# Kernel optimization log

Hardware: AMD Instinct MI355X
Metric: run time of the kernel (lower is better)

Reference implementation:

```python
import jax, jax.numpy as jnp
import numpy as np

N, B, I = 64, 32, 1
EMBED, ACT, DETER, STOCH, HIDDEN = 1536, 16, 2048, 512, 1024
EPS = 1e-5


def _ln(x, g, b):
    m = jnp.mean(x, -1, keepdims=True)
    v = jnp.mean((x - m) ** 2, -1, keepdims=True)
    return (x - m) / jnp.sqrt(v + EPS) * g + b


def setup_inputs() -> dict:
    key = jax.random.key(0)
    ks = jax.random.split(key, 24)
    s = 0.02
    d = {
        "embed": jax.random.normal(ks[0], (N, B, EMBED), jnp.float32),
        "action": jax.random.normal(ks[1], (N, B, ACT), jnp.float32),
        "reset": jnp.zeros((N, B), jnp.bool_),
        "h0": jnp.zeros((B * I, DETER), jnp.float32),
        "z0": jnp.zeros((B * I, STOCH), jnp.float32),
        "noises": jax.random.normal(ks[2], (N, B, I, STOCH), jnp.float32),
        # params
        "W_z": jax.random.normal(ks[3], (HIDDEN, STOCH)) * s,
        "b_z": jnp.zeros((HIDDEN,)),
        "W_a": jax.random.normal(ks[4], (HIDDEN, ACT)) * s,
        "ln_in_g": jnp.ones((HIDDEN,)), "ln_in_b": jnp.zeros((HIDDEN,)),
        "gru_Wih": jax.random.normal(ks[5], (3 * DETER, HIDDEN)) * s,
        "gru_Whh": jax.random.normal(ks[6], (3 * DETER, DETER)) * s,
        "gru_bih": jnp.zeros((3 * DETER,)), "gru_bhh": jnp.zeros((3 * DETER,)),
        "W_ph": jax.random.normal(ks[7], (HIDDEN, DETER)) * s,
        "b_ph": jnp.zeros((HIDDEN,)),
        "W_pe": jax.random.normal(ks[8], (HIDDEN, EMBED)) * s,
        "ln_post_g": jnp.ones((HIDDEN,)), "ln_post_b": jnp.zeros((HIDDEN,)),
        "W_post": jax.random.normal(ks[9], (2 * STOCH, HIDDEN)) * s,
        "b_post": jnp.zeros((2 * STOCH,)),
        "W_prh": jax.random.normal(ks[10], (HIDDEN, DETER)) * s,
        "b_prh": jnp.zeros((HIDDEN,)),
        "ln_pr_g": jnp.ones((HIDDEN,)), "ln_pr_b": jnp.zeros((HIDDEN,)),
        "W_pr": jax.random.normal(ks[11], (2 * STOCH, HIDDEN)) * s,
        "b_pr": jnp.zeros((2 * STOCH,)),
    }
    return d


def _core(embed, action, reset, h0, z0, noises,
          W_z, b_z, W_a, ln_in_g, ln_in_b,
          gru_Wih, gru_Whh, gru_bih, gru_bhh,
          W_ph, b_ph, W_pe, ln_post_g, ln_post_b, W_post, b_post,
          W_prh, b_prh, ln_pr_g, ln_pr_b, W_pr, b_pr):
    n, b = embed.shape[:2]
    # expand to (n, b*I, .) ; I == 1
    embeds = embed.reshape(n, b * I, -1)
    actions = action.reshape(n, b * I, -1)
    masks = (~reset).astype(jnp.float32).reshape(n, b * I, 1)
    noise = noises.reshape(n, b * I, -1)

    def step(carry, xs):
        h, z = carry
        e_t, a_t, m_t, n_t = xs
        h = h * m_t
        z = z * m_t
        x = z @ W_z.T + b_z + a_t @ W_a.T
        za = jax.nn.elu(_ln(x, ln_in_g, ln_in_b))
        # torch GRUCell
        gi = za @ gru_Wih.T + gru_bih
        gh = h @ gru_Whh.T + gru_bhh
        gi_r, gi_u, gi_n = jnp.split(gi, 3, -1)
        gh_r, gh_u, gh_n = jnp.split(gh, 3, -1)
        r = jax.nn.sigmoid(gi_r + gh_r)
        u = jax.nn.sigmoid(gi_u + gh_u)
        cand = jnp.tanh(gi_n + r * gh_n)
        h_new = (1.0 - u) * cand + u * h
        x = h_new @ W_ph.T + b_ph + e_t @ W_pe.T
        post_in = jax.nn.elu(_ln(x, ln_post_g, ln_post_b))
        post = post_in @ W_post.T + b_post
        mean, std_raw = jnp.split(post, 2, -1)
        std = jax.nn.softplus(std_raw) + 0.1
        sample = mean + std * n_t
        return (h_new, sample), (post, h_new, sample)

    (h_last, z_last), (posts, states_h, samples) = jax.lax.scan(
        step, (h0, z0), (embeds, actions, masks, noise))

    # batch prior over all h
    x = states_h @ W_prh.T + b_prh
    x = jax.nn.elu(_ln(x, ln_pr_g, ln_pr_b))
    priors = x @ W_pr.T + b_pr
    features = jnp.concatenate([states_h, samples], -1)

    rs = lambda t: t.reshape(n, b, I, -1)
    return rs(priors), rs(posts), rs(samples), rs(features), h_last, z_last


def reference(embed, action, reset, h0, z0, noises,
              W_z, b_z, W_a, ln_in_g, ln_in_b,
              gru_Wih, gru_Whh, gru_bih, gru_bhh,
              W_ph, b_ph, W_pe, ln_post_g, ln_post_b, W_post, b_post,
              W_prh, b_prh, ln_pr_g, ln_pr_b, W_pr, b_pr):
    return _core(embed, action, reset, h0, z0, noises,
                 W_z, b_z, W_a, ln_in_g, ln_in_b,
                 gru_Wih, gru_Whh, gru_bih, gru_bhh,
                 W_ph, b_ph, W_pe, ln_post_g, ln_post_b, W_post, b_post,
                 W_prh, b_prh, ln_pr_g, ln_pr_b, W_pr, b_pr)
```

## Files before the change

### kernel.cpp

```cpp
#include <hip/hip_runtime.h>
#include <hip/hip_bf16.h>
#include <stdint.h>

#define NSTEP 64
#define BATCH 32
#define EMBED_D 1536
#define ACT_D 16
#define DETER 2048
#define STOCH 512
#define HIDDEN 1024
#define FEAT 2560
#define NBLK 256

typedef __attribute__((ext_vector_type(8))) short bf16x8;
typedef __attribute__((ext_vector_type(4))) float f32x4;

#define MFMA16 __builtin_amdgcn_mfma_f32_16x16x32_bf16
#define AGENT __HIP_MEMORY_SCOPE_AGENT

__device__ __forceinline__ float eluf(float x) { return x > 0.f ? x : expf(x) - 1.f; }
__device__ __forceinline__ float sigf(float x) { return 1.f / (1.f + expf(-x)); }
__device__ __forceinline__ unsigned short f2bf(float f) {
    __hip_bfloat16 h = __float2bfloat16(f);
    return __builtin_bit_cast(unsigned short, h);
}
__device__ __forceinline__ float bf2f(unsigned short u) {
    unsigned v = ((unsigned)u) << 16;
    return __builtin_bit_cast(float, v);
}

__device__ __forceinline__ void stc_u32(unsigned* p, unsigned v) {
    __hip_atomic_store(p, v, __ATOMIC_RELAXED, AGENT);
}
__device__ __forceinline__ void stc_u64(unsigned long long* p, unsigned long long v) {
    __hip_atomic_store(p, v, __ATOMIC_RELAXED, AGENT);
}
__device__ __forceinline__ unsigned long long ldc_u64(const unsigned long long* p) {
    return __hip_atomic_load(p, __ATOMIC_RELAXED, AGENT);
}
__device__ __forceinline__ float ldc_f32(const float* p) {
    return __hip_atomic_load(p, __ATOMIC_RELAXED, AGENT);
}
__device__ __forceinline__ int ldc_i32(const int* p) {
    return __hip_atomic_load(p, __ATOMIC_RELAXED, AGENT);
}
__device__ __forceinline__ void stc_i32(int* p, int v) {
    __hip_atomic_store(p, v, __ATOMIC_RELAXED, AGENT);
}
__device__ __forceinline__ bf16x8 ldc_bf8(const unsigned short* p) {
    union { unsigned long long q[2]; bf16x8 v; } u;
    u.q[0] = ldc_u64((const unsigned long long*)p);
    u.q[1] = ldc_u64((const unsigned long long*)(p + 4));
    return u.v;
}
__device__ __forceinline__ ushort4 ldc_us4(const unsigned short* p) {
    unsigned long long q = ldc_u64((const unsigned long long*)p);
    return __builtin_bit_cast(ushort4, q);
}

__device__ __forceinline__ void gbar2(int* flags, int* release, int epoch) {
    asm volatile("s_waitcnt vmcnt(0)" ::: "memory");
    __syncthreads();
    if (blockIdx.x == 0) {
        int tid = threadIdx.x;
        if (tid >= 1 && tid < NBLK) {
            while (ldc_i32(&flags[tid * 32]) < epoch) __builtin_amdgcn_s_sleep(4);
        }
        asm volatile("" ::: "memory");
        __syncthreads();
        if (tid == 0) stc_i32(release, epoch);
    } else {
        if (threadIdx.x == 0) {
            stc_i32(&flags[blockIdx.x * 32], epoch);
            while (ldc_i32(release) < epoch) __builtin_amdgcn_s_sleep(4);
        }
        asm volatile("" ::: "memory");
        __syncthreads();
    }
}

__global__ __launch_bounds__(256) void k_cvt_all(
    const float* __restrict__ s0, unsigned short* __restrict__ d0,
    const float* __restrict__ s1, unsigned short* __restrict__ d1,
    const float* __restrict__ s2, unsigned short* __restrict__ d2,
    const float* __restrict__ s3, unsigned short* __restrict__ d3,
    const float* __restrict__ s4, unsigned short* __restrict__ d4)
{
    long long e = ((long long)blockIdx.x * 256 + threadIdx.x) * 4;
    const float* src; unsigned short* dst; long long off;
    if (e < 524288)        { src = s0; dst = d0; off = e; }
    else if (e < 6815744)  { src = s1; dst = d1; off = e - 524288; }
    else if (e < 19398656) { src = s2; dst = d2; off = e - 6815744; }
    else if (e < 21495808) { src = s3; dst = d3; off = e - 19398656; }
    else if (e < 22544384) { src = s4; dst = d4; off = e - 21495808; }
    else return;
    float4 v = *reinterpret_cast<const float4*>(src + off);
    ushort4 o;
    o.x = f2bf(v.x); o.y = f2bf(v.y); o.z = f2bf(v.z); o.w = f2bf(v.w);
    *reinterpret_cast<ushort4*>(dst + off) = o;
}

__global__ __launch_bounds__(256) void k_setup(
    const float* __restrict__ h0, const float* __restrict__ z0,
    const uint8_t* __restrict__ reset0,
    float* __restrict__ h0m, unsigned short* __restrict__ h16m0,
    unsigned short* __restrict__ z16m, int* __restrict__ flags)
{
    int gid = blockIdx.x * 256 + threadIdx.x;
    int idx = gid * 4;
    if (idx < BATCH * DETER) {
        int b = idx >> 11;
        float m = reset0[b] ? 0.f : 1.f;
        float4 v = *reinterpret_cast<const float4*>(h0 + idx);
        v.x *= m; v.y *= m; v.z *= m; v.w *= m;
        *reinterpret_cast<float4*>(h0m + idx) = v;
        ushort4 o;
        o.x = f2bf(v.x); o.y = f2bf(v.y); o.z = f2bf(v.z); o.w = f2bf(v.w);
        *reinterpret_cast<ushort4*>(h16m0 + idx) = o;
    } else if (idx < BATCH * DETER + BATCH * STOCH) {
        int zi = idx - BATCH * DETER;
        int b = zi >> 9;
        float m = reset0[b] ? 0.f : 1.f;
        float4 v = *reinterpret_cast<const float4*>(z0 + zi);
        ushort4 o;
        o.x = f2bf(v.x * m); o.y = f2bf(v.y * m); o.z = f2bf(v.z * m); o.w = f2bf(v.w * m);
        *reinterpret_cast<ushort4*>(z16m + zi) = o;
    }
    if (gid < 8224) flags[gid] = 0;
}

__global__ __launch_bounds__(256) void k_preA(
    const float* __restrict__ action, const float* __restrict__ Wa,
    const float* __restrict__ bz, float* __restrict__ preA)
{
    __shared__ float al[16];
    int r = blockIdx.x, t = threadIdx.x;
    if (t < 16) al[t] = action[r * 16 + t];
    __syncthreads();
#pragma unroll
    for (int c = 0; c < 4; ++c) {
        int j = t + c * 256;
        const float* wr = Wa + j * 16;
        float s = bz[j];
#pragma unroll
        for (int k = 0; k < 16; ++k) s += al[k] * wr[k];
        preA[(size_t)r * 1024 + j] = s;
    }
}

__global__ __launch_bounds__(256) void gemm_mfma(
    const float* __restrict__ A, int lda,
    const float* __restrict__ B, int ldb,
    const float* __restrict__ bias,
    float* __restrict__ C, int ldc, int K)
{
    __shared__ unsigned short Alds[64 * 72];
    __shared__ unsigned short Blds[64 * 72];
    int t = threadIdx.x;
    int nb = blockIdx.x, mb = blockIdx.y;
    int w = t >> 6, l = t & 63, l15 = l & 15, kg = l >> 4;
    f32x4 acc[4] = {{0,0,0,0},{0,0,0,0},{0,0,0,0},{0,0,0,0}};
    int srow = t >> 2, skq = (t & 3) * 16;
    const float* Asrc = A + (size_t)(mb * 64 + srow) * lda + skq;
    const float* Bsrc = B + (size_t)(nb * 64 + srow) * ldb + skq;
    unsigned short* Adst = &Alds[srow * 72 + skq];
    unsigned short* Bdst = &Blds[srow * 72 + skq];
    for (int kt = 0; kt < K; kt += 64) {
        __syncthreads();
#pragma unroll
        for (int c = 0; c < 16; c += 4) {
            float4 va = *reinterpret_cast<const float4*>(Asrc + kt + c);
            float4 vb = *reinterpret_cast<const float4*>(Bsrc + kt + c);
            ushort4 oa, ob;
            oa.x = f2bf(va.x); oa.y = f2bf(va.y); oa.z = f2bf(va.z); oa.w = f2bf(va.w);
            ob.x = f2bf(vb.x); ob.y = f2bf(vb.y); ob.z = f2bf(vb.z); ob.w = f2bf(vb.w);
            *reinterpret_cast<ushort4*>(Adst + c) = oa;
            *reinterpret_cast<ushort4*>(Bdst + c) = ob;
        }
        __syncthreads();
#pragma unroll
        for (int ks = 0; ks < 2; ks++) {
            bf16x8 a = *reinterpret_cast<const bf16x8*>(&Alds[(w * 16 + l15) * 72 + ks * 32 + kg * 8]);
#pragma unroll
            for (int nt = 0; nt < 4; nt++) {
                bf16x8 b = *reinterpret_cast<const bf16x8*>(&Blds[(nt * 16 + l15) * 72 + ks * 32 + kg * 8]);
                acc[nt] = MFMA16(a, b, acc[nt], 0, 0, 0);
            }
        }
    }
#pragma unroll
    for (int nt = 0; nt < 4; nt++) {
        int n = nb * 64 + nt * 16 + l15;
        float bv = bias[n];
#pragma unroll
        for (int i = 0; i < 4; i++) {
            C[(size_t)(mb * 64 + w * 16 + kg * 4 + i) * ldc + n] = acc[nt][i] + bv;
        }
    }
}

__global__ __launch_bounds__(256) void ln_elu_rows(
    float* __restrict__ X, const float* __restrict__ g, const float* __restrict__ bb)
{
    __shared__ float sbuf[256], qbuf[256];
    int r = blockIdx.x, t = threadIdx.x;
    float* row = X + (size_t)r * HIDDEN;
    float4 v = reinterpret_cast<const float4*>(row)[t];
    sbuf[t] = (v.x + v.y) + (v.z + v.w);
    qbuf[t] = (v.x * v.x + v.y * v.y) + (v.z * v.z + v.w * v.w);
    __syncthreads();
    for (int off = 128; off > 0; off >>= 1) {
        if (t < off) { sbuf[t] += sbuf[t + off]; qbuf[t] += qbuf[t + off]; }
        __syncthreads();
    }
    float mean = sbuf[0] / HIDDEN;
    float var = qbuf[0] / HIDDEN - mean * mean;
    float rstd = rsqrtf(var + 1e-5f);
    float4 gg = reinterpret_cast<const float4*>(g)[t];
    float4 bv = reinterpret_cast<const float4*>(bb)[t];
    float4 o;
    o.x = eluf((v.x - mean) * rstd * gg.x + bv.x);
    o.y = eluf((v.y - mean) * rstd * gg.y + bv.y);
    o.z = eluf((v.z - mean) * rstd * gg.z + bv.z);
    o.w = eluf((v.w - mean) * rstd * gg.w + bv.w);
    reinterpret_cast<float4*>(row)[t] = o;
}

__global__ __launch_bounds__(256) void k_copy_last(
    const float* __restrict__ feat63, const float* __restrict__ samp63,
    float* __restrict__ hlast, float* __restrict__ zlast)
{
    int i = blockIdx.x * 256 + threadIdx.x;
    if (i < BATCH * DETER) {
        int b = i / DETER, k = i % DETER;
        hlast[i] = feat63[(size_t)b * FEAT + k];
    }
    if (i < BATCH * STOCH) zlast[i] = samp63[i];
}

struct ScanArgs {
    const unsigned short *Wz16, *Wih16, *Whh16, *Wph16, *Wpo16;
    const float *bih, *bhh, *b_post;
    const float *ln_in_g, *ln_in_b, *ln_post_g, *ln_post_b;
    const float *h0m;
    const uint8_t *reset;
    const float *noises;
    float *postsPreA;
    float *priorsPreE;
    float *samples;
    float *feats;
    unsigned short *z16m, *x1b, *x2b, *h16u, *h16m0, *h16m1;
    float *x1parts, *x2parts;
    int *flags, *release;
};

__device__ __forceinline__ void ln_stats(const float* __restrict__ parts, float* stat, int tid) {
    if (tid < 32) {
        float s = 0.f, q = 0.f;
        for (int i = 0; i < 64; ++i) {
            union { unsigned long long u; float f[2]; } c;
            c.u = ldc_u64((const unsigned long long*)(parts + (size_t)(i * 32 + tid) * 2));
            s += c.f[0]; q += c.f[1];
        }
        float mean = s * (1.f / 1024.f);
        float var = q * (1.f / 1024.f) - mean * mean;
        stat[tid] = mean;
        stat[32 + tid] = rsqrtf(var + 1e-5f);
    }
}

__device__ __forceinline__ void ln_fill(unsigned short* Asm, const unsigned short* __restrict__ src,
                                        const float* __restrict__ g, const float* __restrict__ bb,
                                        const float* stat, int tid) {
    int row = tid & 31, kb = (tid >> 5) * 128;
    float mean = stat[row], rstd = stat[32 + row];
#pragma unroll 4
    for (int c = 0; c < 16; ++c) {
        int k = kb + c * 8;
        ushort4 u0 = ldc_us4(src + (size_t)row * 1024 + k);
        ushort4 u1 = ldc_us4(src + (size_t)row * 1024 + k + 4);
        float4 g0 = *reinterpret_cast<const float4*>(g + k);
        float4 g1 = *reinterpret_cast<const float4*>(g + k + 4);
        float4 b0 = *reinterpret_cast<const float4*>(bb + k);
        float4 b1 = *reinterpret_cast<const float4*>(bb + k + 4);
        ushort4 o0, o1;
        o0.x = f2bf(eluf((bf2f(u0.x) - mean) * rstd * g0.x + b0.x));
        o0.y = f2bf(eluf((bf2f(u0.y) - mean) * rstd * g0.y + b0.y));
        o0.z = f2bf(eluf((bf2f(u0.z) - mean) * rstd * g0.z + b0.z));
        o0.w = f2bf(eluf((bf2f(u0.w) - mean) * rstd * g0.w + b0.w));
        o1.x = f2bf(eluf((bf2f(u1.x) - mean) * rstd * g1.x + b1.x));
        o1.y = f2bf(eluf((bf2f(u1.y) - mean) * rstd * g1.y + b1.y));
        o1.z = f2bf(eluf((bf2f(u1.z) - mean) * rstd * g1.z + b1.z));
        o1.w = f2bf(eluf((bf2f(u1.w) - mean) * rstd * g1.w + b1.w));
        *reinterpret_cast<ushort4*>(Asm + row * 1032 + k) = o0;
        *reinterpret_cast<ushort4*>(Asm + row * 1032 + k + 4) = o1;
    }
}

__global__ __launch_bounds__(256, 1) void k_scan(ScanArgs a) {
    __shared__ char smem[74752];
    unsigned short* Asm = (unsigned short*)smem;
    float* cbuf = (float*)(smem + 66048);
    float* stat = (float*)(smem + 66048 + 8192);

    const int bid = blockIdx.x;
    const int tid = threadIdx.x;
    const int w = tid >> 6, l = tid & 63, l15 = l & 15, kg = l >> 4;
    int epoch = 0;

    for (int t = 0; t < NSTEP; ++t) {
        const float* preA_t = a.postsPreA + (size_t)t * 32768;
        const float* preE_t = a.priorsPreE + (size_t)t * 32768;
        float* posts_t = a.postsPreA + (size_t)t * 32768;
        float* samples_t = a.samples + (size_t)t * 16384;
        float* feats_t = a.feats + (size_t)t * 81920;
        const float* featsPrev = a.feats + (size_t)(t - 1) * 81920;
        const unsigned short* h16cur = (t & 1) ? a.h16m1 : a.h16m0;
        unsigned short* h16nxt = (t & 1) ? a.h16m0 : a.h16m1;

        if (bid < 64) {
            int j0 = bid * 16;
            const unsigned short* A0 = a.z16m + l15 * 512 + w * 128 + kg * 8;
            const unsigned short* A1 = A0 + 16 * 512;
            const unsigned short* Bp = a.Wz16 + (size_t)(j0 + l15) * 512 + w * 128 + kg * 8;
            f32x4 c0 = {0,0,0,0}, c1 = {0,0,0,0};
#pragma unroll
            for (int ks = 0; ks < 4; ++ks) {
                bf16x8 b = *reinterpret_cast<const bf16x8*>(Bp + ks * 32);
                c0 = MFMA16(ldc_bf8(A0 + ks * 32), b, c0, 0, 0, 0);
                c1 = MFMA16(ldc_bf8(A1 + ks * 32), b, c1, 0, 0, 0);
            }
#pragma unroll
            for (int i = 0; i < 4; ++i) {
                cbuf[w * 512 + (kg * 4 + i) * 16 + l15] = c0[i];
                cbuf[w * 512 + (16 + kg * 4 + i) * 16 + l15] = c1[i];
            }
            __syncthreads();
            int r = tid >> 3, c2 = (tid & 7) * 2;
            int base = r * 16 + c2;
            float v0 = cbuf[base] + cbuf[512 + base] + cbuf[1024 + base] + cbuf[1536 + base]
                     + preA_t[r * 1024 + j0 + c2];
            float v1 = cbuf[base + 1] + cbuf[512 + base + 1] + cbuf[1024 + base + 1] + cbuf[1536 + base + 1]
                     + preA_t[r * 1024 + j0 + c2 + 1];
            unsigned short u0 = f2bf(v0), u1 = f2bf(v1);
            stc_u32((unsigned*)(a.x1b + (size_t)r * 1024 + j0 + c2),
                    (unsigned)u0 | ((unsigned)u1 << 16));
            float w0 = bf2f(u0), w1 = bf2f(u1);
            float s = w0 + w1, q = w0 * w0 + w1 * w1;
            s += __shfl_xor(s, 1); q += __shfl_xor(q, 1);
            s += __shfl_xor(s, 2); q += __shfl_xor(q, 2);
            s += __shfl_xor(s, 4); q += __shfl_xor(q, 4);
            if ((tid & 7) == 0) {
                union { float f[2]; unsigned long long u; } pu;
                pu.f[0] = s; pu.f[1] = q;
                stc_u64((unsigned long long*)(a.x1parts + ((size_t)bid * 32 + r) * 2), pu.u);
            }
        }
        epoch++; gbar2(a.flags, a.release, epoch);

        if (bid < 128) {
            int j0 = bid * 16;
            ln_stats(a.x1parts, stat, tid);
            __syncthreads();
            ln_fill(Asm, a.x1b, a.ln_in_g, a.ln_in_b, stat, tid);
            __syncthreads();
            bool isI = (w < 2);
            int mt = w & 1;
            f32x4 cr = {0,0,0,0}, cu = {0,0,0,0}, cn = {0,0,0,0};
            if (isI) {
                const unsigned short* ap = Asm + (mt * 16 + l15) * 1032 + kg * 8;
                const unsigned short* br = a.Wih16 + (size_t)(j0 + l15) * 1024 + kg * 8;
                const unsigned short* bu = br + (size_t)2048 * 1024;
                const unsigned short* bn = bu + (size_t)2048 * 1024;
#pragma unroll 8
                for (int ks = 0; ks < 32; ++ks) {
                    bf16x8 av = *reinterpret_cast<const bf16x8*>(ap + ks * 32);
                    cr = MFMA16(av, *reinterpret_cast<const bf16x8*>(br + ks * 32), cr, 0, 0, 0);
                    cu = MFMA16(av, *reinterpret_cast<const bf16x8*>(bu + ks * 32), cu, 0, 0, 0);
                    cn = MFMA16(av, *reinterpret_cast<const bf16x8*>(bn + ks * 32), cn, 0, 0, 0);
                }
            } else {
                const unsigned short* ap = h16cur + (size_t)(mt * 16 + l15) * 2048 + kg * 8;
                const unsigned short* br = a.Whh16 + (size_t)(j0 + l15) * 2048 + kg * 8;
                const unsigned short* bu = br + (size_t)2048 * 2048;
                const unsigned short* bn = bu + (size_t)2048 * 2048;
#pragma unroll 8
                for (int ks = 0; ks < 64; ++ks) {
                    bf16x8 av = ldc_bf8(ap + ks * 32);
                    cr = MFMA16(av, *reinterpret_cast<const bf16x8*>(br + ks * 32), cr, 0, 0, 0);
                    cu = MFMA16(av, *reinterpret_cast<const bf16x8*>(bu + ks * 32), cu, 0, 0, 0);
                    cn = MFMA16(av, *reinterpret_cast<const bf16x8*>(bn + ks * 32), cn, 0, 0, 0);
                }
#pragma unroll
                for (int i = 0; i < 4; ++i) {
                    cbuf[((mt * 3 + 0) * 16 + kg * 4 + i) * 16 + l15] = cr[i];
                    cbuf[((mt * 3 + 1) * 16 + kg * 4 + i) * 16 + l15] = cu[i];
                    cbuf[((mt * 3 + 2) * 16 + kg * 4 + i) * 16 + l15] = cn[i];
                }
            }
            __syncthreads();
            if (isI) {
                int j = j0 + l15;
                float bihr = a.bih[j], bihu = a.bih[j + 2048], bihn = a.bih[j + 4096];
                float bhhr = a.bhh[j], bhhu = a.bhh[j + 2048], bhhn = a.bhh[j + 4096];
#pragma unroll
                for (int i = 0; i < 4; ++i) {
                    int b = mt * 16 + kg * 4 + i;
                    float gr = cr[i] + bihr, gu = cu[i] + bihu, gn = cn[i] + bihn;
                    float hr = cbuf[((mt * 3 + 0) * 16 + kg * 4 + i) * 16 + l15] + bhhr;
                    float hu = cbuf[((mt * 3 + 1) * 16 + kg * 4 + i) * 16 + l15] + bhhu;
                    float hn = cbuf[((mt * 3 + 2) * 16 + kg * 4 + i) * 16 + l15] + bhhn;
                    float r = sigf(gr + hr), u = sigf(gu + hu);
                    float cand = tanhf(gn + r * hn);
                    float m = a.reset[t * 32 + b] ? 0.f : 1.f;
                    float hpv = (t == 0) ? a.h0m[b * 2048 + j]
                                         : ldc_f32(featsPrev + (size_t)b * 2560 + j);
                    float hnew = (1.f - u) * cand + u * (m * hpv);
                    cbuf[1536 + b * 16 + l15] = hnew;
                }
            }
            __syncthreads();
            {
                int b = tid >> 3, c2 = (tid & 7) * 2;
                float h0v = cbuf[1536 + b * 16 + c2], h1v = cbuf[1536 + b * 16 + c2 + 1];
                int j = j0 + c2;
                union { float f[2]; unsigned long long u; } fu;
                fu.f[0] = h0v; fu.f[1] = h1v;
                stc_u64((unsigned long long*)(feats_t + (size_t)b * 2560 + j), fu.u);
                unsigned short g0 = f2bf(h0v), g1 = f2bf(h1v);
                stc_u32((unsigned*)(a.h16u + (size_t)b * 2048 + j),
                        (unsigned)g0 | ((unsigned)g1 << 16));
                float mn = (t < 63) ? (a.reset[(t + 1) * 32 + b] ? 0.f : 1.f) : 1.f;
                unsigned short n0 = f2bf(h0v * mn), n1 = f2bf(h1v * mn);
                stc_u32((unsigned*)(h16nxt + (size_t)b * 2048 + j),
                        (unsigned)n0 | ((unsigned)n1 << 16));
            }
        }
        epoch++; gbar2(a.flags, a.release, epoch);

        if (bid < 64) {
            int j0 = bid * 16;
            const unsigned short* A0 = a.h16u + l15 * 2048 + w * 512 + kg * 8;
            const unsigned short* A1 = A0 + 16 * 2048;
            const unsigned short* Bp = a.Wph16 + (size_t)(j0 + l15) * 2048 + w * 512 + kg * 8;
            f32x4 c0 = {0,0,0,0}, c1 = {0,0,0,0};
#pragma unroll 8
            for (int ks = 0; ks < 16; ++ks) {
                bf16x8 b = *reinterpret_cast<const bf16x8*>(Bp + ks * 32);
                c0 = MFMA16(ldc_bf8(A0 + ks * 32), b, c0, 0, 0, 0);
                c1 = MFMA16(ldc_bf8(A1 + ks * 32), b, c1, 0, 0, 0);
            }
#pragma unroll
            for (int i = 0; i < 4; ++i) {
                cbuf[w * 512 + (kg * 4 + i) * 16 + l15] = c0[i];
                cbuf[w * 512 + (16 + kg * 4 + i) * 16 + l15] = c1[i];
            }
            __syncthreads();
            int r = tid >> 3, c2 = (tid & 7) * 2;
            int base = r * 16 + c2;
            float v0 = cbuf[base] + cbuf[512 + base] + cbuf[1024 + base] + cbuf[1536 + base]
                     + preE_t[r * 1024 + j0 + c2];
            float v1 = cbuf[base + 1] + cbuf[512 + base + 1] + cbuf[1024 + base + 1] + cbuf[1536 + base + 1]
                     + preE_t[r * 1024 + j0 + c2 + 1];
            unsigned short u0 = f2bf(v0), u1 = f2bf(v1);
            stc_u32((unsigned*)(a.x2b + (size_t)r * 1024 + j0 + c2),
                    (unsigned)u0 | ((unsigned)u1 << 16));
            float w0 = bf2f(u0), w1 = bf2f(u1);
            float s = w0 + w1, q = w0 * w0 + w1 * w1;
            s += __shfl_xor(s, 1); q += __shfl_xor(q, 1);
            s += __shfl_xor(s, 2); q += __shfl_xor(q, 2);
            s += __shfl_xor(s, 4); q += __shfl_xor(q, 4);
            if ((tid & 7) == 0) {
                union { float f[2]; unsigned long long u; } pu;
                pu.f[0] = s; pu.f[1] = q;
                stc_u64((unsigned long long*)(a.x2parts + ((size_t)bid * 32 + r) * 2), pu.u);
            }
        }
        epoch++; gbar2(a.flags, a.release, epoch);

        if (bid < 32) {
            int j0 = bid * 16;
            ln_stats(a.x2parts, stat, tid);
            __syncthreads();
            ln_fill(Asm, a.x2b, a.ln_post_g, a.ln_post_b, stat, tid);
            __syncthreads();
            int tile = w >> 1, mt = w & 1;
            const unsigned short* ap = Asm + (mt * 16 + l15) * 1032 + kg * 8;
            int n = (tile == 0) ? (j0 + l15) : (512 + j0 + l15);
            const unsigned short* Bp = a.Wpo16 + (size_t)n * 1024 + kg * 8;
            f32x4 c = {0,0,0,0};
#pragma unroll 8
            for (int ks = 0; ks < 32; ++ks) {
                c = MFMA16(*reinterpret_cast<const bf16x8*>(ap + ks * 32),
                           *reinterpret_cast<const bf16x8*>(Bp + ks * 32), c, 0, 0, 0);
            }
#pragma unroll
            for (int i = 0; i < 4; ++i)
                cbuf[(tile * 2 + mt) * 256 + (kg * 4 + i) * 16 + l15] = c[i];
            __syncthreads();
            int b = tid >> 3, c2 = (tid & 7) * 2;
            int j = j0 + c2;
            int ib = (b >> 4) * 256 + (b & 15) * 16;
            float pm0 = cbuf[ib + c2] + a.b_post[j];
            float pm1 = cbuf[ib + c2 + 1] + a.b_post[j + 1];
            float ps0 = cbuf[512 + ib + c2] + a.b_post[512 + j];
            float ps1 = cbuf[512 + ib + c2 + 1] + a.b_post[512 + j + 1];
            posts_t[(size_t)b * 1024 + j] = pm0;
            posts_t[(size_t)b * 1024 + j + 1] = pm1;
            posts_t[(size_t)b * 1024 + 512 + j] = ps0;
            posts_t[(size_t)b * 1024 + 512 + j + 1] = ps1;
            float sp0 = fmaxf(ps0, 0.f) + log1pf(expf(-fabsf(ps0)));
            float sp1 = fmaxf(ps1, 0.f) + log1pf(expf(-fabsf(ps1)));
            float n0v = a.noises[(size_t)t * 16384 + b * 512 + j];
            float n1v = a.noises[(size_t)t * 16384 + b * 512 + j + 1];
            float smp0 = pm0 + (sp0 + 0.1f) * n0v;
            float smp1 = pm1 + (sp1 + 0.1f) * n1v;
            samples_t[(size_t)b * 512 + j] = smp0;
            samples_t[(size_t)b * 512 + j + 1] = smp1;
            feats_t[(size_t)b * 2560 + 2048 + j] = smp0;
            feats_t[(size_t)b * 2560 + 2048 + j + 1] = smp1;
            float mn = (t < 63) ? (a.reset[(t + 1) * 32 + b] ? 0.f : 1.f) : 1.f;
            unsigned short z0_ = f2bf(smp0 * mn), z1_ = f2bf(smp1 * mn);
            stc_u32((unsigned*)(a.z16m + (size_t)b * 512 + j),
                    (unsigned)z0_ | ((unsigned)z1_ << 16));
        }
        epoch++; gbar2(a.flags, a.release, epoch);
    }
}

#define WS_WZ16   ((size_t)0)
#define WS_WIH16  ((size_t)1048576)
#define WS_WHH16  ((size_t)13631488)
#define WS_WPH16  ((size_t)38797312)
#define WS_WPO16  ((size_t)42991616)
#define WS_Z16M   ((size_t)45088768)
#define WS_H16M0  ((size_t)45121536)
#define WS_H16M1  ((size_t)45252608)
#define WS_H16U   ((size_t)45383680)
#define WS_H0M    ((size_t)45514752)
#define WS_X1B    ((size_t)45776896)
#define WS_X2B    ((size_t)45842432)
#define WS_X1P    ((size_t)45907968)
#define WS_X2P    ((size_t)45924352)
#define WS_FLAGS  ((size_t)45940736)
#define WS_REL    ((size_t)45973504)
#define WS_PRX    WS_WIH16

extern "C" void kernel_launch(void* const* d_in, const int* in_sizes, int n_in,
                              void* d_out, int out_size, void* d_ws, size_t ws_size,
                              hipStream_t stream)
{
    (void)in_sizes; (void)n_in; (void)out_size; (void)ws_size;
    const float*   embed  = (const float*)d_in[0];
    const float*   action = (const float*)d_in[1];
    const uint8_t* reset  = (const uint8_t*)d_in[2];
    const float*   h0     = (const float*)d_in[3];
    const float*   z0     = (const float*)d_in[4];
    const float*   noises = (const float*)d_in[5];
    const float*   W_z    = (const float*)d_in[6];
    const float*   b_z    = (const float*)d_in[7];
    const float*   W_a    = (const float*)d_in[8];
    const float*   ln_in_g = (const float*)d_in[9];
    const float*   ln_in_b = (const float*)d_in[10];
    const float*   Wih    = (const float*)d_in[11];
    const float*   Whh    = (const float*)d_in[12];
    const float*   bih    = (const float*)d_in[13];
    const float*   bhh    = (const float*)d_in[14];
    const float*   W_ph   = (const float*)d_in[15];
    const float*   b_ph   = (const float*)d_in[16];
    const float*   W_pe   = (const float*)d_in[17];
    const float*   ln_post_g = (const float*)d_in[18];
    const float*   ln_post_b = (const float*)d_in[19];
    const float*   W_post = (const float*)d_in[20];
    const float*   b_post = (const float*)d_in[21];
    const float*   W_prh  = (const float*)d_in[22];
    const float*   b_prh  = (const float*)d_in[23];
    const float*   ln_pr_g = (const float*)d_in[24];
    const float*   ln_pr_b = (const float*)d_in[25];
    const float*   W_pr   = (const float*)d_in[26];
    const float*   b_pr   = (const float*)d_in[27];

    float* out     = (float*)d_out;
    float* priors  = out;
    float* posts   = out + 2097152;
    float* samples = out + 4194304;
    float* feats   = out + 5242880;
    float* hlast   = out + 10485760;
    float* zlast   = out + 10551296;

    char* ws = (char*)d_ws;
    unsigned short* Wz16  = (unsigned short*)(ws + WS_WZ16);
    unsigned short* Wih16 = (unsigned short*)(ws + WS_WIH16);
    unsigned short* Whh16 = (unsigned short*)(ws + WS_WHH16);
    unsigned short* Wph16 = (unsigned short*)(ws + WS_WPH16);
    unsigned short* Wpo16 = (unsigned short*)(ws + WS_WPO16);
    unsigned short* z16m  = (unsigned short*)(ws + WS_Z16M);
    unsigned short* h16m0 = (unsigned short*)(ws + WS_H16M0);
    unsigned short* h16m1 = (unsigned short*)(ws + WS_H16M1);
    unsigned short* h16u  = (unsigned short*)(ws + WS_H16U);
    float*          h0m   = (float*)(ws + WS_H0M);
    unsigned short* x1b   = (unsigned short*)(ws + WS_X1B);
    unsigned short* x2b   = (unsigned short*)(ws + WS_X2B);
    float*          x1p   = (float*)(ws + WS_X1P);
    float*          x2p   = (float*)(ws + WS_X2P);
    int*            flags = (int*)(ws + WS_FLAGS);
    int*            release = (int*)(ws + WS_REL);
    float*          prx   = (float*)(ws + WS_PRX);

    dim3 blk(256);

    k_cvt_all<<<dim3(22016), blk, 0, stream>>>(W_z, Wz16, Wih, Wih16, Whh, Whh16,
                                               W_ph, Wph16, W_post, Wpo16);
    k_setup<<<dim3(80), blk, 0, stream>>>(h0, z0, reset, h0m, h16m0, z16m, flags);

    k_preA<<<dim3(2048), blk, 0, stream>>>(action, W_a, b_z, posts);
    gemm_mfma<<<dim3(16, 32), blk, 0, stream>>>(embed, EMBED_D, W_pe, EMBED_D, b_ph,
                                                priors, HIDDEN, EMBED_D);

    ScanArgs sa;
    sa.Wz16 = Wz16; sa.Wih16 = Wih16; sa.Whh16 = Whh16; sa.Wph16 = Wph16; sa.Wpo16 = Wpo16;
    sa.bih = bih; sa.bhh = bhh; sa.b_post = b_post;
    sa.ln_in_g = ln_in_g; sa.ln_in_b = ln_in_b; sa.ln_post_g = ln_post_g; sa.ln_post_b = ln_post_b;
    sa.h0m = h0m; sa.reset = reset; sa.noises = noises;
    sa.postsPreA = posts; sa.priorsPreE = priors; sa.samples = samples; sa.feats = feats;
    sa.z16m = z16m; sa.x1b = x1b; sa.x2b = x2b; sa.h16u = h16u;
    sa.h16m0 = h16m0; sa.h16m1 = h16m1;
    sa.x1parts = x1p; sa.x2parts = x2p;
    sa.flags = flags; sa.release = release;
    void* kp[] = { (void*)&sa };
    hipLaunchCooperativeKernel((const void*)k_scan, dim3(NBLK), blk, kp, 0, stream);

    gemm_mfma<<<dim3(16, 32), blk, 0, stream>>>(feats, FEAT, W_prh, DETER, b_prh,
                                                prx, HIDDEN, DETER);
    ln_elu_rows<<<dim3(2048), blk, 0, stream>>>(prx, ln_pr_g, ln_pr_b);
    gemm_mfma<<<dim3(16, 32), blk, 0, stream>>>(prx, HIDDEN, W_pr, HIDDEN, b_pr,
                                                priors, HIDDEN, HIDDEN);

    k_copy_last<<<dim3(256), blk, 0, stream>>>(
        feats + (size_t)(NSTEP - 1) * BATCH * FEAT,
        samples + (size_t)(NSTEP - 1) * BATCH * STOCH,
        hlast, zlast);
}
```

Baseline: 4.744 ms.

## Store recurrent GRU and posterior weights as scaled FP8, dequantize in loop

Converts Wih, Whh and Wph to e4m3 FP8 with a fixed ×1024 scale instead of bf16. Inside the persistent scan kernel the FP8 bytes are expanded to bf16 before each MFMA, and the outputs are rescaled. This halves the bytes streamed per recurrent step, which matters because the scan re-reads these weights every step. The cost is extra conversion ALU work and FP8 quantization error on the weights, which may hurt accuracy against the fp32 reference.

Result: slower. 5.478 ms (+15.5%).

```diff
diff --git a/kernel.cpp b/kernel.cpp
--- a/kernel.cpp
+++ b/kernel.cpp
@@ -1,5 +1,6 @@
 #include <hip/hip_runtime.h>
 #include <hip/hip_bf16.h>
+#include <hip/hip_fp8.h>
 #include <stdint.h>
 
 #define NSTEP 64
@@ -17,6 +18,7 @@
 
 #define MFMA16 __builtin_amdgcn_mfma_f32_16x16x32_bf16
 #define AGENT __HIP_MEMORY_SCOPE_AGENT
+#define INV8 (1.0f / 1024.0f)
 
 __device__ __forceinline__ float eluf(float x) { return x > 0.f ? x : expf(x) - 1.f; }
 __device__ __forceinline__ float sigf(float x) { return 1.f / (1.f + expf(-x)); }
@@ -27,6 +29,39 @@
 __device__ __forceinline__ float bf2f(unsigned short u) {
     unsigned v = ((unsigned)u) << 16;
     return __builtin_bit_cast(float, v);
+}
+
+template <int SEL>
+__device__ __forceinline__ float fp8_to_f32(unsigned u) {
+#if __has_builtin(__builtin_amdgcn_cvt_f32_fp8)
+    return __builtin_amdgcn_cvt_f32_fp8(u, SEL);
+#else
+    __hip_fp8_e4m3 q; q.__x = (unsigned char)(u >> (SEL * 8));
+    return (float)q;
+#endif
+}
+__device__ __forceinline__ unsigned char f32_to_fp8(float x) {
+    x = fminf(fmaxf(x, -448.f), 448.f);
+#if __has_builtin(__builtin_amdgcn_cvt_pk_fp8_f32)
+    int r = __builtin_amdgcn_cvt_pk_fp8_f32(x, x, 0, false);
+    return (unsigned char)(r & 0xff);
+#else
+    __hip_fp8_e4m3 q(x);
+    return q.__x;
+#endif
+}
+__device__ __forceinline__ bf16x8 dq8(const unsigned char* p) {
+    uint2 d = *reinterpret_cast<const uint2*>(p);
+    union { unsigned short s[8]; bf16x8 o; } u;
+    u.s[0] = f2bf(fp8_to_f32<0>(d.x));
+    u.s[1] = f2bf(fp8_to_f32<1>(d.x));
+    u.s[2] = f2bf(fp8_to_f32<2>(d.x));
+    u.s[3] = f2bf(fp8_to_f32<3>(d.x));
+    u.s[4] = f2bf(fp8_to_f32<0>(d.y));
+    u.s[5] = f2bf(fp8_to_f32<1>(d.y));
+    u.s[6] = f2bf(fp8_to_f32<2>(d.y));
+    u.s[7] = f2bf(fp8_to_f32<3>(d.y));
+    return u.o;
 }
 
 __device__ __forceinline__ void stc_u32(unsigned* p, unsigned v) {
@@ -80,24 +115,36 @@
 }
 
 __global__ __launch_bounds__(256) void k_cvt_all(
-    const float* __restrict__ s0, unsigned short* __restrict__ d0,
-    const float* __restrict__ s1, unsigned short* __restrict__ d1,
-    const float* __restrict__ s2, unsigned short* __restrict__ d2,
-    const float* __restrict__ s3, unsigned short* __restrict__ d3,
-    const float* __restrict__ s4, unsigned short* __restrict__ d4)
+    const float* __restrict__ wz, unsigned short* __restrict__ wz16,
+    const float* __restrict__ wpo, unsigned short* __restrict__ wpo16,
+    const float* __restrict__ wih, unsigned char* __restrict__ wih8,
+    const float* __restrict__ whh, unsigned char* __restrict__ whh8,
+    const float* __restrict__ wph, unsigned char* __restrict__ wph8)
 {
     long long e = ((long long)blockIdx.x * 256 + threadIdx.x) * 4;
-    const float* src; unsigned short* dst; long long off;
-    if (e < 524288)        { src = s0; dst = d0; off = e; }
-    else if (e < 6815744)  { src = s1; dst = d1; off = e - 524288; }
-    else if (e < 19398656) { src = s2; dst = d2; off = e - 6815744; }
-    else if (e < 21495808) { src = s3; dst = d3; off = e - 19398656; }
-    else if (e < 22544384) { src = s4; dst = d4; off = e - 21495808; }
-    else return;
-    float4 v = *reinterpret_cast<const float4*>(src + off);
-    ushort4 o;
-    o.x = f2bf(v.x); o.y = f2bf(v.y); o.z = f2bf(v.z); o.w = f2bf(v.w);
-    *reinterpret_cast<ushort4*>(dst + off) = o;
+    if (e < 1572864) {
+        const float* src; unsigned short* dst; long long off;
+        if (e < 524288) { src = wz;  dst = wz16;  off = e; }
+        else            { src = wpo; dst = wpo16; off = e - 524288; }
+        float4 v = *reinterpret_cast<const float4*>(src + off);
+        ushort4 o;
+        o.x = f2bf(v.x); o.y = f2bf(v.y); o.z = f2bf(v.z); o.w = f2bf(v.w);
+        *reinterpret_cast<ushort4*>(dst + off) = o;
+    } else {
+        long long f = e - 1572864;
+        const float* src; unsigned char* dst; long long off;
+        if (f < 6291456)        { src = wih; dst = wih8; off = f; }
+        else if (f < 18874368)  { src = whh; dst = whh8; off = f - 6291456; }
+        else if (f < 20971520)  { src = wph; dst = wph8; off = f - 18874368; }
+        else return;
+        float4 v = *reinterpret_cast<const float4*>(src + off);
+        uchar4 o;
+        o.x = f32_to_fp8(v.x * 1024.f);
+        o.y = f32_to_fp8(v.y * 1024.f);
+        o.z = f32_to_fp8(v.z * 1024.f);
+        o.w = f32_to_fp8(v.w * 1024.f);
+        *reinterpret_cast<uchar4*>(dst + off) = o;
+    }
 }
 
 __global__ __launch_bounds__(256) void k_setup(
@@ -239,7 +286,8 @@
 }
 
 struct ScanArgs {
-    const unsigned short *Wz16, *Wih16, *Whh16, *Wph16, *Wpo16;
+    const unsigned short *Wz16, *Wpo16;
+    const unsigned char *Wih8, *Whh8, *Wph8;
     const float *bih, *bhh, *b_post;
     const float *ln_in_g, *ln_in_b, *ln_post_g, *ln_post_b;
     const float *h0m;
@@ -369,27 +417,27 @@
             f32x4 cr = {0,0,0,0}, cu = {0,0,0,0}, cn = {0,0,0,0};
             if (isI) {
                 const unsigned short* ap = Asm + (mt * 16 + l15) * 1032 + kg * 8;
-                const unsigned short* br = a.Wih16 + (size_t)(j0 + l15) * 1024 + kg * 8;
-                const unsigned short* bu = br + (size_t)2048 * 1024;
-                const unsigned short* bn = bu + (size_t)2048 * 1024;
+                const unsigned char* br = a.Wih8 + (size_t)(j0 + l15) * 1024 + kg * 8;
+                const unsigned char* bu = br + (size_t)2048 * 1024;
+                const unsigned char* bn = bu + (size_t)2048 * 1024;
 #pragma unroll 8
                 for (int ks = 0; ks < 32; ++ks) {
                     bf16x8 av = *reinterpret_cast<const bf16x8*>(ap + ks * 32);
-                    cr = MFMA16(av, *reinterpret_cast<const bf16x8*>(br + ks * 32), cr, 0, 0, 0);
-                    cu = MFMA16(av, *reinterpret_cast<const bf16x8*>(bu + ks * 32), cu, 0, 0, 0);
-                    cn = MFMA16(av, *reinterpret_cast<const bf16x8*>(bn + ks * 32), cn, 0, 0, 0);
+                    cr = MFMA16(av, dq8(br + ks * 32), cr, 0, 0, 0);
+                    cu = MFMA16(av, dq8(bu + ks * 32), cu, 0, 0, 0);
+                    cn = MFMA16(av, dq8(bn + ks * 32), cn, 0, 0, 0);
                 }
             } else {
                 const unsigned short* ap = h16cur + (size_t)(mt * 16 + l15) * 2048 + kg * 8;
-                const unsigned short* br = a.Whh16 + (size_t)(j0 + l15) * 2048 + kg * 8;
-                const unsigned short* bu = br + (size_t)2048 * 2048;
-                const unsigned short* bn = bu + (size_t)2048 * 2048;
+                const unsigned char* br = a.Whh8 + (size_t)(j0 + l15) * 2048 + kg * 8;
+                const unsigned char* bu = br + (size_t)2048 * 2048;
+                const unsigned char* bn = bu + (size_t)2048 * 2048;
 #pragma unroll 8
                 for (int ks = 0; ks < 64; ++ks) {
                     bf16x8 av = ldc_bf8(ap + ks * 32);
-                    cr = MFMA16(av, *reinterpret_cast<const bf16x8*>(br + ks * 32), cr, 0, 0, 0);
-                    cu = MFMA16(av, *reinterpret_cast<const bf16x8*>(bu + ks * 32), cu, 0, 0, 0);
-                    cn = MFMA16(av, *reinterpret_cast<const bf16x8*>(bn + ks * 32), cn, 0, 0, 0);
+                    cr = MFMA16(av, dq8(br + ks * 32), cr, 0, 0, 0);
+                    cu = MFMA16(av, dq8(bu + ks * 32), cu, 0, 0, 0);
+                    cn = MFMA16(av, dq8(bn + ks * 32), cn, 0, 0, 0);
                 }
 #pragma unroll
                 for (int i = 0; i < 4; ++i) {
@@ -406,10 +454,12 @@
 #pragma unroll
                 for (int i = 0; i < 4; ++i) {
                     int b = mt * 16 + kg * 4 + i;
-                    float gr = cr[i] + bihr, gu = cu[i] + bihu, gn = cn[i] + bihn;
-                    float hr = cbuf[((mt * 3 + 0) * 16 + kg * 4 + i) * 16 + l15] + bhhr;
-                    float hu = cbuf[((mt * 3 + 1) * 16 + kg * 4 + i) * 16 + l15] + bhhu;
-                    float hn = cbuf[((mt * 3 + 2) * 16 + kg * 4 + i) * 16 + l15] + bhhn;
+                    float gr = cr[i] * INV8 + bihr;
+                    float gu = cu[i] * INV8 + bihu;
+                    float gn = cn[i] * INV8 + bihn;
+                    float hr = cbuf[((mt * 3 + 0) * 16 + kg * 4 + i) * 16 + l15] * INV8 + bhhr;
+                    float hu = cbuf[((mt * 3 + 1) * 16 + kg * 4 + i) * 16 + l15] * INV8 + bhhu;
+                    float hn = cbuf[((mt * 3 + 2) * 16 + kg * 4 + i) * 16 + l15] * INV8 + bhhn;
                     float r = sigf(gr + hr), u = sigf(gu + hu);
                     float cand = tanhf(gn + r * hn);
                     float m = a.reset[t * 32 + b] ? 0.f : 1.f;
@@ -442,11 +492,11 @@
             int j0 = bid * 16;
             const unsigned short* A0 = a.h16u + l15 * 2048 + w * 512 + kg * 8;
             const unsigned short* A1 = A0 + 16 * 2048;
-            const unsigned short* Bp = a.Wph16 + (size_t)(j0 + l15) * 2048 + w * 512 + kg * 8;
+            const unsigned char* Bp = a.Wph8 + (size_t)(j0 + l15) * 2048 + w * 512 + kg * 8;
             f32x4 c0 = {0,0,0,0}, c1 = {0,0,0,0};
 #pragma unroll 8
             for (int ks = 0; ks < 16; ++ks) {
-                bf16x8 b = *reinterpret_cast<const bf16x8*>(Bp + ks * 32);
+                bf16x8 b = dq8(Bp + ks * 32);
                 c0 = MFMA16(ldc_bf8(A0 + ks * 32), b, c0, 0, 0, 0);
                 c1 = MFMA16(ldc_bf8(A1 + ks * 32), b, c1, 0, 0, 0);
             }
@@ -458,9 +508,9 @@
             __syncthreads();
             int r = tid >> 3, c2 = (tid & 7) * 2;
             int base = r * 16 + c2;
-            float v0 = cbuf[base] + cbuf[512 + base] + cbuf[1024 + base] + cbuf[1536 + base]
+            float v0 = (cbuf[base] + cbuf[512 + base] + cbuf[1024 + base] + cbuf[1536 + base]) * INV8
                      + preE_t[r * 1024 + j0 + c2];
-            float v1 = cbuf[base + 1] + cbuf[512 + base + 1] + cbuf[1024 + base + 1] + cbuf[1536 + base + 1]
+            float v1 = (cbuf[base + 1] + cbuf[512 + base + 1] + cbuf[1024 + base + 1] + cbuf[1536 + base + 1]) * INV8
                      + preE_t[r * 1024 + j0 + c2 + 1];
             unsigned short u0 = f2bf(v0), u1 = f2bf(v1);
             stc_u32((unsigned*)(a.x2b + (size_t)r * 1024 + j0 + c2),
@@ -529,22 +579,22 @@
 }
 
 #define WS_WZ16   ((size_t)0)
-#define WS_WIH16  ((size_t)1048576)
-#define WS_WHH16  ((size_t)13631488)
-#define WS_WPH16  ((size_t)38797312)
-#define WS_WPO16  ((size_t)42991616)
-#define WS_Z16M   ((size_t)45088768)
-#define WS_H16M0  ((size_t)45121536)
-#define WS_H16M1  ((size_t)45252608)
-#define WS_H16U   ((size_t)45383680)
-#define WS_H0M    ((size_t)45514752)
-#define WS_X1B    ((size_t)45776896)
-#define WS_X2B    ((size_t)45842432)
-#define WS_X1P    ((size_t)45907968)
-#define WS_X2P    ((size_t)45924352)
-#define WS_FLAGS  ((size_t)45940736)
-#define WS_REL    ((size_t)45973504)
-#define WS_PRX    WS_WIH16
+#define WS_WIH8   ((size_t)1048576)
+#define WS_WHH8   ((size_t)7340032)
+#define WS_WPH8   ((size_t)19922944)
+#define WS_WPO16  ((size_t)22020096)
+#define WS_Z16M   ((size_t)24117248)
+#define WS_H16M0  ((size_t)24150016)
+#define WS_H16M1  ((size_t)24281088)
+#define WS_H16U   ((size_t)24412160)
+#define WS_H0M    ((size_t)24543232)
+#define WS_X1B    ((size_t)24805376)
+#define WS_X2B    ((size_t)24870912)
+#define WS_X1P    ((size_t)24936448)
+#define WS_X2P    ((size_t)24952832)
+#define WS_FLAGS  ((size_t)24969216)
+#define WS_REL    ((size_t)25001984)
+#define WS_PRX    WS_WIH8
 
 extern "C" void kernel_launch(void* const* d_in, const int* in_sizes, int n_in,
                               void* d_out, int out_size, void* d_ws, size_t ws_size,
@@ -590,9 +640,9 @@
 
     char* ws = (char*)d_ws;
     unsigned short* Wz16  = (unsigned short*)(ws + WS_WZ16);
-    unsigned short* Wih16 = (unsigned short*)(ws + WS_WIH16);
-    unsigned short* Whh16 = (unsigned short*)(ws + WS_WHH16);
-    unsigned short* Wph16 = (unsigned short*)(ws + WS_WPH16);
+    unsigned char*  Wih8  = (unsigned char*)(ws + WS_WIH8);
+    unsigned char*  Whh8  = (unsigned char*)(ws + WS_WHH8);
+    unsigned char*  Wph8  = (unsigned char*)(ws + WS_WPH8);
     unsigned short* Wpo16 = (unsigned short*)(ws + WS_WPO16);
     unsigned short* z16m  = (unsigned short*)(ws + WS_Z16M);
     unsigned short* h16m0 = (unsigned short*)(ws + WS_H16M0);
@@ -609,8 +659,8 @@
 
     dim3 blk(256);
 
-    k_cvt_all<<<dim3(22016), blk, 0, stream>>>(W_z, Wz16, Wih, Wih16, Whh, Whh16,
-                                               W_ph, Wph16, W_post, Wpo16);
+    k_cvt_all<<<dim3(22016), blk, 0, stream>>>(W_z, Wz16, W_post, Wpo16,
+                                               Wih, Wih8, Whh, Whh8, W_ph, Wph8);
     k_setup<<<dim3(80), blk, 0, stream>>>(h0, z0, reset, h0m, h16m0, z16m, flags);
 
     k_preA<<<dim3(2048), blk, 0, stream>>>(action, W_a, b_z, posts);
@@ -618,7 +668,8 @@
                                                 priors, HIDDEN, EMBED_D);
 
     ScanArgs sa;
-    sa.Wz16 = Wz16; sa.Wih16 = Wih16; sa.Whh16 = Whh16; sa.Wph16 = Wph16; sa.Wpo16 = Wpo16;
+    sa.Wz16 = Wz16; sa.Wpo16 = Wpo16;
+    sa.Wih8 = Wih8; sa.Whh8 = Whh8; sa.Wph8 = Wph8;
     sa.bih = bih; sa.bhh = bhh; sa.b_post = b_post;
     sa.ln_in_g = ln_in_g; sa.ln_in_b = ln_in_b; sa.ln_post_g = ln_post_g; sa.ln_post_b = ln_post_b;
     sa.h0m = h0m; sa.reset = reset; sa.noises = noises;
@@ -628,7 +679,7 @@
     sa.x1parts = x1p; sa.x2parts = x2p;
     sa.flags = flags; sa.release = release;
     void* kp[] = { (void*)&sa };
-    hipLaunchCooperativeKernel((const void*)k_scan, dim3(NBLK), blk, kp, 0, stream);
+    (void)hipLaunchCooperativeKernel((const void*)k_scan, dim3(NBLK), blk, kp, 0, stream);
 
     gemm_mfma<<<dim3(16, 32), blk, 0, stream>>>(feats, FEAT, W_prh, DETER, b_prh,
                                                 prx, HIDDEN, DETER);
```
